# Optimization experiments

Measured on AMD Instinct MI355X. Metric: run time of the kernel, lower is better.

## Reference

```python
import jax, jax.numpy as jnp
import numpy as np

B, S, D, H = 1, 2048, 1024, 16
DH = D // H  # 64
ROPE_THETA = 10000.0


def _rope_tables(seq_len, half_dim, theta):
    inv = 1.0 / (theta ** (np.arange(0, half_dim, dtype=np.float32) / half_dim))
    ang = np.arange(seq_len, dtype=np.float32)[:, None] * inv[None, :]
    return jnp.asarray(np.cos(ang)), jnp.asarray(np.sin(ang))


def setup_inputs() -> dict:
    key = jax.random.key(0)
    ks = jax.random.split(key, 6)
    x = jax.random.normal(ks[0], (B, S, D), dtype=jnp.float32)
    # block-diagonal mask over ~4 packed images -> sorted segment ids
    seg_ids = jnp.sort(jax.random.randint(ks[1], (S,), 0, 4, dtype=jnp.int32))
    freqs_cos, freqs_sin = _rope_tables(S, DH // 2, ROPE_THETA)
    scale = 1.0 / np.sqrt(D)
    wq = jax.random.normal(ks[2], (D, D), dtype=jnp.float32) * scale
    wk = jax.random.normal(ks[3], (D, D), dtype=jnp.float32) * scale
    wv = jax.random.normal(ks[4], (D, D), dtype=jnp.float32) * scale
    wo = jax.random.normal(ks[5], (D, D), dtype=jnp.float32) * scale
    return {"x": x, "seg_ids": seg_ids, "freqs_cos": freqs_cos,
            "freqs_sin": freqs_sin, "wq": wq, "wk": wk, "wv": wv, "wo": wo}


def _apply_rope(t, cos, sin):
    # t: [B,S,H,DH]; interpret last dim as DH//2 complex pairs (real, imag)
    tr = t.reshape(B, S, H, DH // 2, 2)
    a, b = tr[..., 0], tr[..., 1]
    c = cos[None, :, None, :]  # [1,S,1,DH/2]
    s = sin[None, :, None, :]
    out = jnp.stack([a * c - b * s, a * s + b * c], axis=-1)
    return out.reshape(B, S, H, DH)


def reference(x, seg_ids, freqs_cos, freqs_sin, wq, wk, wv, wo):
    q = (x @ wq.T).reshape(B, S, H, DH)
    k = (x @ wk.T).reshape(B, S, H, DH)
    v = (x @ wv.T).reshape(B, S, H, DH)
    q = _apply_rope(q, freqs_cos, freqs_sin)
    k = _apply_rope(k, freqs_cos, freqs_sin)
    scores = jnp.einsum('bqhd,bkhd->bhqk', q, k) / np.float32(np.sqrt(DH))
    block_mask = (seg_ids[:, None] == seg_ids[None, :])  # [S,S] block-diagonal
    scores = jnp.where(block_mask[None, None], scores, jnp.float32(-1e9))
    attn = jax.nn.softmax(scores, axis=-1)
    out = jnp.einsum('bhqk,bkhd->bqhd', attn, v).reshape(B, S, D)
    return out @ wo.T
```

## Files before the change

kernel.cpp:

```cpp
#include <hip/hip_runtime.h>

typedef __bf16 bf16;
typedef __bf16 bf16x4 __attribute__((ext_vector_type(4)));
typedef __bf16 bf16x8 __attribute__((ext_vector_type(8)));
typedef float  f32x4  __attribute__((ext_vector_type(4)));

#define S_LEN 2048
#define D_DIM 1024
#define NHEAD 16
#define DHEAD 64

__device__ __forceinline__ void async_cp16(const bf16* g, bf16* l) {
  __builtin_amdgcn_global_load_lds(
      (__attribute__((address_space(1))) void*)(void*)g,
      (__attribute__((address_space(3))) void*)l,
      16, 0, 0);
}

__global__ __launch_bounds__(256) void cvt_k(
    const float* __restrict__ x,  const float* __restrict__ w0,
    const float* __restrict__ w1, const float* __restrict__ w2,
    const float* __restrict__ w3, bf16* __restrict__ dst,
    const int* __restrict__ seg, int* __restrict__ kbr)
{
  __shared__ int firstv[4];
  const int b = blockIdx.x;
  const int t = threadIdx.x;

  if (b < 3072) {
    int i = b * 256 + t;
    const float* src;
    int off;
    if (i < (1 << 18)) {
      src = x; off = i;
    } else {
      int j = i - (1 << 18);
      int s = j >> 17;
      off = j & ((1 << 17) - 1);
      src = (s == 0) ? w0 : (s == 1) ? w1 : (s == 2) ? w2 : w3;
    }
    f32x4 a = *(const f32x4*)(src + (size_t)off * 8);
    f32x4 bb = *(const f32x4*)(src + (size_t)off * 8 + 4);
    bf16x8 o;
    o[0] = (bf16)a[0];  o[1] = (bf16)a[1];  o[2] = (bf16)a[2];  o[3] = (bf16)a[3];
    o[4] = (bf16)bb[0]; o[5] = (bf16)bb[1]; o[6] = (bf16)bb[2]; o[7] = (bf16)bb[3];
    *((bf16x8*)dst + i) = o;
  } else {
    if (t < 4) firstv[t] = S_LEN;
    __syncthreads();
    for (int i = t; i < S_LEN; i += 256) {
      int s = seg[i];
      if (i == 0 || seg[i - 1] != s) atomicMin(&firstv[s], i);
    }
    __syncthreads();
    if (t < 32) {
      int smin = seg[t * 64], smax = seg[t * 64 + 63];
      int lb = S_LEN, ub = S_LEN;
      for (int vv = smin; vv < 4; ++vv) lb = min(lb, firstv[vv]);
      for (int vv = smax + 1; vv < 4; ++vv) ub = min(ub, firstv[vv]);
      kbr[t * 2] = lb >> 6;
      kbr[t * 2 + 1] = (ub - 1) >> 6;
    }
  }
}

__global__ __launch_bounds__(256) void gemm_qkv(
    const bf16* __restrict__ A,
    const bf16* __restrict__ B0, const bf16* __restrict__ B1,
    const bf16* __restrict__ B2,
    const float* __restrict__ cosT, const float* __restrict__ sinT,
    bf16* __restrict__ Cbase, bf16* __restrict__ Vt)
{
  constexpr int K = 1024, N = 1024;
  const int z = blockIdx.z;
  const bf16* W = (z == 0) ? B0 : (z == 1) ? B1 : B2;
  bf16* C = Cbase + (size_t)z * 2048 * 1024;

  __shared__ bf16 As[4][128 * 32] __attribute__((aligned(16)));
  __shared__ bf16 Bs[4][64 * 32] __attribute__((aligned(16)));

  const int t = threadIdx.x;
  const int lane = t & 63;
  const int w = t >> 6;
  const int lm = lane & 15, lq = lane >> 4;
  const int wr = w >> 1, wc = w & 1;
  const int bm = blockIdx.y, bn = blockIdx.x;

  const bf16* Abase = A + (size_t)bm * 128 * K;
  const bf16* Wbase = W + (size_t)bn * 64 * K;

  f32x4 acc[4][2] = {};

  for (int kk = 0; kk < K; kk += 128) {
#pragma unroll
    for (int kh = 0; kh < 2; ++kh)
#pragma unroll
      for (int g = 0; g < 2; ++g) {
        int c = (w * 2 + g) * 64 + lane;
        int row = c >> 2, k8 = c & 3;
        const bf16* ga = Abase + (size_t)row * K + kk + kh * 64 + k8 * 8;
        async_cp16(ga, &As[kh * 2][(w * 2 + g) * 512]);
        async_cp16(ga + 32, &As[kh * 2 + 1][(w * 2 + g) * 512]);
      }
#pragma unroll
    for (int kh = 0; kh < 2; ++kh) {
      int c = w * 64 + lane;
      int row = c >> 2, k8 = c & 3;
      const bf16* gb = Wbase + (size_t)row * K + kk + kh * 64 + k8 * 8;
      async_cp16(gb, &Bs[kh * 2][w * 512]);
      async_cp16(gb + 32, &Bs[kh * 2 + 1][w * 512]);
    }
    __syncthreads();

#pragma unroll
    for (int ks = 0; ks < 4; ++ks) {
      bf16x8 af[4], bfr[2];
#pragma unroll
      for (int mi = 0; mi < 4; ++mi)
        af[mi] = *(const bf16x8*)&As[ks][(wr * 64 + mi * 16 + lm) * 32 + lq * 8];
#pragma unroll
      for (int ni = 0; ni < 2; ++ni)
        bfr[ni] = *(const bf16x8*)&Bs[ks][(wc * 32 + ni * 16 + lm) * 32 + lq * 8];
#pragma unroll
      for (int mi = 0; mi < 4; ++mi)
#pragma unroll
        for (int ni = 0; ni < 2; ++ni)
          acc[mi][ni] = __builtin_amdgcn_mfma_f32_16x16x32_bf16(
              af[mi], bfr[ni], acc[mi][ni], 0, 0, 0);
    }
    __syncthreads();
  }

  if (z < 2) {
    const float scale = (z == 0) ? 0.125f : 1.0f;
#pragma unroll
    for (int mi = 0; mi < 4; ++mi)
#pragma unroll
      for (int ni = 0; ni < 2; ++ni) {
        int gcol = bn * 64 + wc * 32 + ni * 16 + lm;
        int p = (gcol & 63) >> 1;
        bool even = (gcol & 1) == 0;
#pragma unroll
        for (int r = 0; r < 4; ++r) {
          int row = bm * 128 + wr * 64 + mi * 16 + lq * 4 + r;
          float v = acc[mi][ni][r];
          float mate = __shfl_xor(v, 1);
          float cv = cosT[row * 32 + p];
          float sv = sinT[row * 32 + p];
          float res = even ? (v * cv - mate * sv) : (mate * sv + v * cv);
          C[(size_t)row * N + gcol] = (bf16)(res * scale);
        }
      }
  } else {
#pragma unroll
    for (int mi = 0; mi < 4; ++mi)
#pragma unroll
      for (int ni = 0; ni < 2; ++ni) {
        int gcol = bn * 64 + wc * 32 + ni * 16 + lm;
        int rowb = bm * 128 + wr * 64 + mi * 16 + lq * 4;
        bf16x4 pack;
#pragma unroll
        for (int r = 0; r < 4; ++r) pack[r] = (bf16)acc[mi][ni][r];
        *(bf16x4*)(Vt + (size_t)gcol * S_LEN + rowb) = pack;
      }
  }
}

__global__ __launch_bounds__(256) void gemm_wo(
    const bf16* __restrict__ A, const bf16* __restrict__ W,
    float* __restrict__ C)
{
  constexpr int K = 1024, N = 1024;

  __shared__ bf16 As[4][64 * 32] __attribute__((aligned(16)));
  __shared__ bf16 Bs[4][64 * 32] __attribute__((aligned(16)));

  const int t = threadIdx.x;
  const int lane = t & 63;
  const int w = t >> 6;
  const int lm = lane & 15, lq = lane >> 4;
  const int bn = blockIdx.x, bm = blockIdx.y;

  const bf16* Abase = A + (size_t)bm * 64 * K;
  const bf16* Wbase = W + (size_t)bn * 64 * K;

  f32x4 acc[4] = {};

  for (int kk = 0; kk < K; kk += 128) {
#pragma unroll
    for (int kh = 0; kh < 2; ++kh) {
      int c = w * 64 + lane;
      int row = c >> 2, k8 = c & 3;
      const bf16* ga = Abase + (size_t)row * K + kk + kh * 64 + k8 * 8;
      async_cp16(ga, &As[kh * 2][w * 512]);
      async_cp16(ga + 32, &As[kh * 2 + 1][w * 512]);
      const bf16* gb = Wbase + (size_t)row * K + kk + kh * 64 + k8 * 8;
      async_cp16(gb, &Bs[kh * 2][w * 512]);
      async_cp16(gb + 32, &Bs[kh * 2 + 1][w * 512]);
    }
    __syncthreads();

#pragma unroll
    for (int ks = 0; ks < 4; ++ks) {
      bf16x8 af = *(const bf16x8*)&As[ks][(w * 16 + lm) * 32 + lq * 8];
      bf16x8 bfr[4];
#pragma unroll
      for (int ni = 0; ni < 4; ++ni)
        bfr[ni] = *(const bf16x8*)&Bs[ks][(ni * 16 + lm) * 32 + lq * 8];
#pragma unroll
      for (int ni = 0; ni < 4; ++ni)
        acc[ni] = __builtin_amdgcn_mfma_f32_16x16x32_bf16(
            af, bfr[ni], acc[ni], 0, 0, 0);
    }
    __syncthreads();
  }

#pragma unroll
  for (int ni = 0; ni < 4; ++ni) {
    int col = bn * 64 + ni * 16 + lm;
#pragma unroll
    for (int r = 0; r < 4; ++r) {
      int row = bm * 64 + w * 16 + lq * 4 + r;
      C[(size_t)row * N + col] = acc[ni][r];
    }
  }
}

__global__ __launch_bounds__(512, 2) void attn_k(
    const bf16* __restrict__ Q, const bf16* __restrict__ Kmat,
    const bf16* __restrict__ Vt, const int* __restrict__ seg,
    const int* __restrict__ kbr,
    bf16* __restrict__ AO)
{
  __shared__ bf16 Ks[64 * 72] __attribute__((aligned(16)));
  __shared__ bf16 Vs[64 * 72] __attribute__((aligned(16)));
  __shared__ bf16 Ps[8][16 * 72] __attribute__((aligned(16)));
  __shared__ int segk[64];

  const int h = blockIdx.y;
  const int qt = blockIdx.x;
  const int q0 = qt * 128;
  const int t = threadIdx.x, lane = t & 63, w = t >> 6;
  const int lm = lane & 15, lq = lane >> 4;
  const int qrow = q0 + w * 16;

  const int kb0f = kbr[qt * 4], kb1f = kbr[qt * 4 + 3];

  bf16x8 qf[2];
#pragma unroll
  for (int ks = 0; ks < 2; ++ks)
    qf[ks] = *(const bf16x8*)(Q + (size_t)(qrow + lm) * D_DIM + h * DHEAD +
                              ks * 32 + lq * 8);

  int sq[4];
  float l_i[4];
#pragma unroll
  for (int r = 0; r < 4; ++r) {
    sq[r] = seg[qrow + lq * 4 + r];
    l_i[r] = 0.0f;
  }
  f32x4 o[4] = {};

  const int srow0 = t >> 3, sch = (t & 7) * 8;

  f32x4 pk0, pv0;
  int psg;
  {
    const int k0 = kb0f * 64;
    pk0 = *(const f32x4*)(Kmat + (size_t)(k0 + srow0) * D_DIM + h * DHEAD + sch);
    pv0 = *(const f32x4*)(Vt + (size_t)(h * DHEAD + srow0) * S_LEN + k0 + sch);
    if (t < 64) psg = seg[k0 + t];
  }

  for (int kb = kb0f; kb <= kb1f; ++kb) {
    __syncthreads();
    *(f32x4*)&Ks[srow0 * 72 + sch] = pk0;
    *(f32x4*)&Vs[srow0 * 72 + sch] = pv0;
    if (t < 64) segk[t] = psg;
    __syncthreads();

    if (kb + 1 <= kb1f) {
      const int k0 = (kb + 1) * 64;
      pk0 = *(const f32x4*)(Kmat + (size_t)(k0 + srow0) * D_DIM + h * DHEAD + sch);
      pv0 = *(const f32x4*)(Vt + (size_t)(h * DHEAD + srow0) * S_LEN + k0 + sch);
      if (t < 64) psg = seg[k0 + t];
    }

    f32x4 sa[4] = {};
    __builtin_amdgcn_s_setprio(1);
#pragma unroll
    for (int ks = 0; ks < 2; ++ks) {
      bf16x8 kf[4];
#pragma unroll
      for (int ni = 0; ni < 4; ++ni)
        kf[ni] = *(const bf16x8*)&Ks[(ni * 16 + lm) * 72 + ks * 32 + lq * 8];
#pragma unroll
      for (int ni = 0; ni < 4; ++ni)
        sa[ni] = __builtin_amdgcn_mfma_f32_16x16x32_bf16(qf[ks], kf[ni],
                                                         sa[ni], 0, 0, 0);
    }
    __builtin_amdgcn_s_setprio(0);

    int sk[4];
#pragma unroll
    for (int ni = 0; ni < 4; ++ni) sk[ni] = segk[ni * 16 + lm];

#pragma unroll
    for (int r = 0; r < 4; ++r)
#pragma unroll
      for (int ni = 0; ni < 4; ++ni) {
        float p = (sq[r] == sk[ni]) ? __expf(sa[ni][r]) : 0.0f;
        l_i[r] += p;
        Ps[w][(lq * 4 + r) * 72 + ni * 16 + lm] = (bf16)p;
      }

    __builtin_amdgcn_s_setprio(1);
#pragma unroll
    for (int ks = 0; ks < 2; ++ks) {
      bf16x8 pf = *(const bf16x8*)&Ps[w][lm * 72 + ks * 32 + lq * 8];
      bf16x8 vf[4];
#pragma unroll
      for (int ni = 0; ni < 4; ++ni)
        vf[ni] = *(const bf16x8*)&Vs[(ni * 16 + lm) * 72 + ks * 32 + lq * 8];
#pragma unroll
      for (int ni = 0; ni < 4; ++ni)
        o[ni] = __builtin_amdgcn_mfma_f32_16x16x32_bf16(pf, vf[ni], o[ni],
                                                        0, 0, 0);
    }
    __builtin_amdgcn_s_setprio(0);
  }

#pragma unroll
  for (int r = 0; r < 4; ++r) {
    float l = l_i[r];
    l += __shfl_xor(l, 1);
    l += __shfl_xor(l, 2);
    l += __shfl_xor(l, 4);
    l += __shfl_xor(l, 8);
    float inv = 1.0f / l;
    int row = qrow + lq * 4 + r;
#pragma unroll
    for (int ni = 0; ni < 4; ++ni)
      AO[(size_t)row * D_DIM + h * DHEAD + ni * 16 + lm] =
          (bf16)(o[ni][r] * inv);
  }
}

extern "C" void kernel_launch(void* const* d_in, const int* in_sizes, int n_in,
                              void* d_out, int out_size, void* d_ws,
                              size_t ws_size, hipStream_t stream)
{
  const float* x  = (const float*)d_in[0];
  const int*   sg = (const int*)d_in[1];
  const float* fc = (const float*)d_in[2];
  const float* fs = (const float*)d_in[3];
  const float* wq = (const float*)d_in[4];
  const float* wk = (const float*)d_in[5];
  const float* wv = (const float*)d_in[6];
  const float* wo = (const float*)d_in[7];
  float* out = (float*)d_out;

  const size_t MAT = (size_t)S_LEN * D_DIM;
  const size_t WSZ = (size_t)D_DIM * D_DIM;
  bf16* xb  = (bf16*)d_ws;
  bf16* wqb = xb + MAT;
  bf16* wkb = wqb + WSZ;
  bf16* wvb = wkb + WSZ;
  bf16* wob = wvb + WSZ;
  bf16* q0  = wob + WSZ;
  bf16* k0  = q0 + MAT;
  bf16* vt  = k0 + MAT;
  bf16* ao  = vt + MAT;
  int*  kbr = (int*)(ao + MAT);

  dim3 blk(256);
  cvt_k<<<dim3(3073), blk, 0, stream>>>(x, wq, wk, wv, wo, xb, sg, kbr);
  gemm_qkv<<<dim3(16, 16, 3), blk, 0, stream>>>(xb, wqb, wkb, wvb, fc, fs,
                                                q0, vt);
  attn_k<<<dim3(16, 16), dim3(512), 0, stream>>>(q0, k0, vt, sg, kbr, ao);
  gemm_wo<<<dim3(16, 32), blk, 0, stream>>>(ao, wob, out);
}
```

Measured before the change: 136.8 us.

## Give each attention wave two query sub-tiles and mask by key segment ranges

The attention kernel drops from 512 to 256 threads per block, and each wave now handles 32 query rows as two 16-row sub-tiles. Each K/V fragment read from LDS is reused across two sets of MFMAs. The score MFMA swaps its operand order so P comes out transposed, which allows packed bf16x4 stores into LDS. The per-key segment comparison is replaced by a key-index range test, using per-segment bounds computed in the convert kernel, so the segk shared array and its loads go away. The costs are higher register pressure, lower wave count per block, and an extra shuffle to redistribute the row normaliser.

```diff
diff --git a/kernel.cpp b/kernel.cpp
--- a/kernel.cpp
+++ b/kernel.cpp
@@ -61,6 +61,12 @@
       kbr[t * 2] = lb >> 6;
       kbr[t * 2 + 1] = (ub - 1) >> 6;
     }
+    if (t < 4) {
+      int ubv = S_LEN;
+      for (int u = t + 1; u < 4; ++u) ubv = min(ubv, firstv[u]);
+      kbr[64 + t * 2] = firstv[t];
+      kbr[64 + t * 2 + 1] = ubv;
+    }
   }
 }
 
@@ -226,7 +232,7 @@
   }
 }
 
-__global__ __launch_bounds__(512, 2) void attn_k(
+__global__ __launch_bounds__(256) void attn_k(
     const bf16* __restrict__ Q, const bf16* __restrict__ Kmat,
     const bf16* __restrict__ Vt, const int* __restrict__ seg,
     const int* __restrict__ kbr,
@@ -234,59 +240,63 @@
 {
   __shared__ bf16 Ks[64 * 72] __attribute__((aligned(16)));
   __shared__ bf16 Vs[64 * 72] __attribute__((aligned(16)));
-  __shared__ bf16 Ps[8][16 * 72] __attribute__((aligned(16)));
-  __shared__ int segk[64];
+  __shared__ bf16 Ps[4][2][16 * 72] __attribute__((aligned(16)));
 
   const int h = blockIdx.y;
   const int qt = blockIdx.x;
-  const int q0 = qt * 128;
   const int t = threadIdx.x, lane = t & 63, w = t >> 6;
   const int lm = lane & 15, lq = lane >> 4;
-  const int qrow = q0 + w * 16;
+  const int qbase = qt * 128 + w * 32;
 
   const int kb0f = kbr[qt * 4], kb1f = kbr[qt * 4 + 3];
 
-  bf16x8 qf[2];
-#pragma unroll
-  for (int ks = 0; ks < 2; ++ks)
-    qf[ks] = *(const bf16x8*)(Q + (size_t)(qrow + lm) * D_DIM + h * DHEAD +
-                              ks * 32 + lq * 8);
-
-  int sq[4];
-  float l_i[4];
-#pragma unroll
-  for (int r = 0; r < 4; ++r) {
-    sq[r] = seg[qrow + lq * 4 + r];
-    l_i[r] = 0.0f;
-  }
-  f32x4 o[4] = {};
-
-  const int srow0 = t >> 3, sch = (t & 7) * 8;
-
-  f32x4 pk0, pv0;
-  int psg;
+  bf16x8 qf[2][2];
+  int lb[2], ub[2];
+  float lacc[2] = {0.f, 0.f};
+  f32x4 o[2][4] = {};
+#pragma unroll
+  for (int s = 0; s < 2; ++s) {
+    int qrow = qbase + s * 16 + lm;
+#pragma unroll
+    for (int ks = 0; ks < 2; ++ks)
+      qf[s][ks] = *(const bf16x8*)(Q + (size_t)qrow * D_DIM + h * DHEAD +
+                                   ks * 32 + lq * 8);
+    int sv = seg[qrow];
+    lb[s] = kbr[64 + sv * 2];
+    ub[s] = kbr[64 + sv * 2 + 1];
+  }
+
+  const int srow0 = t >> 3, srow1 = srow0 + 32;
+  const int sch = (t & 7) * 8;
+
+  f32x4 pk0, pk1, pv0, pv1;
   {
     const int k0 = kb0f * 64;
     pk0 = *(const f32x4*)(Kmat + (size_t)(k0 + srow0) * D_DIM + h * DHEAD + sch);
+    pk1 = *(const f32x4*)(Kmat + (size_t)(k0 + srow1) * D_DIM + h * DHEAD + sch);
     pv0 = *(const f32x4*)(Vt + (size_t)(h * DHEAD + srow0) * S_LEN + k0 + sch);
-    if (t < 64) psg = seg[k0 + t];
+    pv1 = *(const f32x4*)(Vt + (size_t)(h * DHEAD + srow1) * S_LEN + k0 + sch);
   }
 
   for (int kb = kb0f; kb <= kb1f; ++kb) {
     __syncthreads();
     *(f32x4*)&Ks[srow0 * 72 + sch] = pk0;
+    *(f32x4*)&Ks[srow1 * 72 + sch] = pk1;
     *(f32x4*)&Vs[srow0 * 72 + sch] = pv0;
-    if (t < 64) segk[t] = psg;
-    __syncthreads();
-
-    if (kb + 1 <= kb1f) {
+    *(f32x4*)&Vs[srow1 * 72 + sch] = pv1;
+    __syncthreads();
+
+    if (kb < kb1f) {
       const int k0 = (kb + 1) * 64;
       pk0 = *(const f32x4*)(Kmat + (size_t)(k0 + srow0) * D_DIM + h * DHEAD + sch);
+      pk1 = *(const f32x4*)(Kmat + (size_t)(k0 + srow1) * D_DIM + h * DHEAD + sch);
       pv0 = *(const f32x4*)(Vt + (size_t)(h * DHEAD + srow0) * S_LEN + k0 + sch);
-      if (t < 64) psg = seg[k0 + t];
-    }
-
-    f32x4 sa[4] = {};
+      pv1 = *(const f32x4*)(Vt + (size_t)(h * DHEAD + srow1) * S_LEN + k0 + sch);
+    }
+
+    const int k0 = kb * 64;
+
+    f32x4 sa[2][4] = {};
     __builtin_amdgcn_s_setprio(1);
 #pragma unroll
     for (int ks = 0; ks < 2; ++ks) {
@@ -295,54 +305,63 @@
       for (int ni = 0; ni < 4; ++ni)
         kf[ni] = *(const bf16x8*)&Ks[(ni * 16 + lm) * 72 + ks * 32 + lq * 8];
 #pragma unroll
-      for (int ni = 0; ni < 4; ++ni)
-        sa[ni] = __builtin_amdgcn_mfma_f32_16x16x32_bf16(qf[ks], kf[ni],
-                                                         sa[ni], 0, 0, 0);
+      for (int s = 0; s < 2; ++s)
+#pragma unroll
+        for (int ni = 0; ni < 4; ++ni)
+          sa[s][ni] = __builtin_amdgcn_mfma_f32_16x16x32_bf16(
+              kf[ni], qf[s][ks], sa[s][ni], 0, 0, 0);
     }
     __builtin_amdgcn_s_setprio(0);
 
-    int sk[4];
-#pragma unroll
-    for (int ni = 0; ni < 4; ++ni) sk[ni] = segk[ni * 16 + lm];
-
-#pragma unroll
-    for (int r = 0; r < 4; ++r)
+#pragma unroll
+    for (int s = 0; s < 2; ++s)
 #pragma unroll
       for (int ni = 0; ni < 4; ++ni) {
-        float p = (sq[r] == sk[ni]) ? __expf(sa[ni][r]) : 0.0f;
-        l_i[r] += p;
-        Ps[w][(lq * 4 + r) * 72 + ni * 16 + lm] = (bf16)p;
+        bf16x4 pk;
+#pragma unroll
+        for (int r = 0; r < 4; ++r) {
+          int key = k0 + ni * 16 + lq * 4 + r;
+          float p = (key >= lb[s] && key < ub[s]) ? __expf(sa[s][ni][r]) : 0.0f;
+          lacc[s] += p;
+          pk[r] = (bf16)p;
+        }
+        *(bf16x4*)&Ps[w][s][lm * 72 + ni * 16 + lq * 4] = pk;
       }
 
     __builtin_amdgcn_s_setprio(1);
 #pragma unroll
     for (int ks = 0; ks < 2; ++ks) {
-      bf16x8 pf = *(const bf16x8*)&Ps[w][lm * 72 + ks * 32 + lq * 8];
       bf16x8 vf[4];
 #pragma unroll
       for (int ni = 0; ni < 4; ++ni)
         vf[ni] = *(const bf16x8*)&Vs[(ni * 16 + lm) * 72 + ks * 32 + lq * 8];
 #pragma unroll
+      for (int s = 0; s < 2; ++s) {
+        bf16x8 pf = *(const bf16x8*)&Ps[w][s][lm * 72 + ks * 32 + lq * 8];
+#pragma unroll
+        for (int ni = 0; ni < 4; ++ni)
+          o[s][ni] = __builtin_amdgcn_mfma_f32_16x16x32_bf16(
+              pf, vf[ni], o[s][ni], 0, 0, 0);
+      }
+    }
+    __builtin_amdgcn_s_setprio(0);
+  }
+
+#pragma unroll
+  for (int s = 0; s < 2; ++s) {
+    float l = lacc[s];
+    l += __shfl_xor(l, 16);
+    l += __shfl_xor(l, 32);
+    float inv = 1.0f / l;
+#pragma unroll
+    for (int r = 0; r < 4; ++r) {
+      float invr = __shfl(inv, lq * 4 + r);
+      int row = qbase + s * 16 + lq * 4 + r;
+#pragma unroll
       for (int ni = 0; ni < 4; ++ni)
-        o[ni] = __builtin_amdgcn_mfma_f32_16x16x32_bf16(pf, vf[ni], o[ni],
-                                                        0, 0, 0);
-    }
-    __builtin_amdgcn_s_setprio(0);
-  }
-
-#pragma unroll
-  for (int r = 0; r < 4; ++r) {
-    float l = l_i[r];
-    l += __shfl_xor(l, 1);
-    l += __shfl_xor(l, 2);
-    l += __shfl_xor(l, 4);
-    l += __shfl_xor(l, 8);
-    float inv = 1.0f / l;
-    int row = qrow + lq * 4 + r;
-#pragma unroll
-    for (int ni = 0; ni < 4; ++ni)
-      AO[(size_t)row * D_DIM + h * DHEAD + ni * 16 + lm] =
-          (bf16)(o[ni][r] * inv);
+        AO[(size_t)row * D_DIM + h * DHEAD + ni * 16 + lm] =
+            (bf16)(o[s][ni][r] * invr);
+    }
   }
 }
 
@@ -377,6 +396,6 @@
   cvt_k<<<dim3(3073), blk, 0, stream>>>(x, wq, wk, wv, wo, xb, sg, kbr);
   gemm_qkv<<<dim3(16, 16, 3), blk, 0, stream>>>(xb, wqb, wkb, wvb, fc, fs,
                                                 q0, vt);
-  attn_k<<<dim3(16, 16), dim3(512), 0, stream>>>(q0, k0, vt, sg, kbr, ao);
+  attn_k<<<dim3(16, 16), blk, 0, stream>>>(q0, k0, vt, sg, kbr, ao);
   gemm_wo<<<dim3(16, 32), blk, 0, stream>>>(ao, wob, out);
 }
```

Result: slower. 143.6 us (+5.0%).

## Load K/V fragments directly from global and mask by segment range bounds

Applied to the files above, without the earlier changes.

Removes the shared-memory staging of K and V tiles and the two block barriers per key block; each wave now loads its MFMA operand fragments straight from global memory. The segment-equality mask is replaced by a per-query-row key range [lb, ub) precomputed in the conversion kernel, which removes the segk LDS array. This trades barrier and LDS traffic for redundant global/L2 loads across the 8 waves and loses the register prefetch of the next tile.

```diff
diff --git a/kernel.cpp b/kernel.cpp
--- a/kernel.cpp
+++ b/kernel.cpp
@@ -61,6 +61,12 @@
       kbr[t * 2] = lb >> 6;
       kbr[t * 2 + 1] = (ub - 1) >> 6;
     }
+    if (t < 4) {
+      int ubv = S_LEN;
+      for (int u = t + 1; u < 4; ++u) ubv = min(ubv, firstv[u]);
+      kbr[64 + t * 2] = firstv[t];
+      kbr[64 + t * 2 + 1] = ubv;
+    }
   }
 }
 
@@ -232,10 +238,7 @@
     const int* __restrict__ kbr,
     bf16* __restrict__ AO)
 {
-  __shared__ bf16 Ks[64 * 72] __attribute__((aligned(16)));
-  __shared__ bf16 Vs[64 * 72] __attribute__((aligned(16)));
   __shared__ bf16 Ps[8][16 * 72] __attribute__((aligned(16)));
-  __shared__ int segk[64];
 
   const int h = blockIdx.y;
   const int qt = blockIdx.x;
@@ -252,39 +255,22 @@
     qf[ks] = *(const bf16x8*)(Q + (size_t)(qrow + lm) * D_DIM + h * DHEAD +
                               ks * 32 + lq * 8);
 
-  int sq[4];
+  int lbq[4], ubq[4];
   float l_i[4];
 #pragma unroll
   for (int r = 0; r < 4; ++r) {
-    sq[r] = seg[qrow + lq * 4 + r];
+    int sv = seg[qrow + lq * 4 + r];
+    lbq[r] = kbr[64 + sv * 2];
+    ubq[r] = kbr[64 + sv * 2 + 1];
     l_i[r] = 0.0f;
   }
   f32x4 o[4] = {};
 
-  const int srow0 = t >> 3, sch = (t & 7) * 8;
-
-  f32x4 pk0, pv0;
-  int psg;
-  {
-    const int k0 = kb0f * 64;
-    pk0 = *(const f32x4*)(Kmat + (size_t)(k0 + srow0) * D_DIM + h * DHEAD + sch);
-    pv0 = *(const f32x4*)(Vt + (size_t)(h * DHEAD + srow0) * S_LEN + k0 + sch);
-    if (t < 64) psg = seg[k0 + t];
-  }
+  const bf16* Kb = Kmat + h * DHEAD;
+  const bf16* Vb = Vt + (size_t)h * DHEAD * S_LEN;
 
   for (int kb = kb0f; kb <= kb1f; ++kb) {
-    __syncthreads();
-    *(f32x4*)&Ks[srow0 * 72 + sch] = pk0;
-    *(f32x4*)&Vs[srow0 * 72 + sch] = pv0;
-    if (t < 64) segk[t] = psg;
-    __syncthreads();
-
-    if (kb + 1 <= kb1f) {
-      const int k0 = (kb + 1) * 64;
-      pk0 = *(const f32x4*)(Kmat + (size_t)(k0 + srow0) * D_DIM + h * DHEAD + sch);
-      pv0 = *(const f32x4*)(Vt + (size_t)(h * DHEAD + srow0) * S_LEN + k0 + sch);
-      if (t < 64) psg = seg[k0 + t];
-    }
+    const int k0 = kb * 64;
 
     f32x4 sa[4] = {};
     __builtin_amdgcn_s_setprio(1);
@@ -293,7 +279,8 @@
       bf16x8 kf[4];
 #pragma unroll
       for (int ni = 0; ni < 4; ++ni)
-        kf[ni] = *(const bf16x8*)&Ks[(ni * 16 + lm) * 72 + ks * 32 + lq * 8];
+        kf[ni] = *(const bf16x8*)(Kb + (size_t)(k0 + ni * 16 + lm) * D_DIM +
+                                  ks * 32 + lq * 8);
 #pragma unroll
       for (int ni = 0; ni < 4; ++ni)
         sa[ni] = __builtin_amdgcn_mfma_f32_16x16x32_bf16(qf[ks], kf[ni],
@@ -301,15 +288,12 @@
     }
     __builtin_amdgcn_s_setprio(0);
 
-    int sk[4];
-#pragma unroll
-    for (int ni = 0; ni < 4; ++ni) sk[ni] = segk[ni * 16 + lm];
-
 #pragma unroll
     for (int r = 0; r < 4; ++r)
 #pragma unroll
       for (int ni = 0; ni < 4; ++ni) {
-        float p = (sq[r] == sk[ni]) ? __expf(sa[ni][r]) : 0.0f;
+        int key = k0 + ni * 16 + lm;
+        float p = (key >= lbq[r] && key < ubq[r]) ? __expf(sa[ni][r]) : 0.0f;
         l_i[r] += p;
         Ps[w][(lq * 4 + r) * 72 + ni * 16 + lm] = (bf16)p;
       }
@@ -321,7 +305,8 @@
       bf16x8 vf[4];
 #pragma unroll
       for (int ni = 0; ni < 4; ++ni)
-        vf[ni] = *(const bf16x8*)&Vs[(ni * 16 + lm) * 72 + ks * 32 + lq * 8];
+        vf[ni] = *(const bf16x8*)(Vb + (size_t)(ni * 16 + lm) * S_LEN +
+                                  k0 + ks * 32 + lq * 8);
 #pragma unroll
       for (int ni = 0; ni < 4; ++ni)
         o[ni] = __builtin_amdgcn_mfma_f32_16x16x32_bf16(pf, vf[ni], o[ni],
```

After: 180.2 us. 31.7% more time.

## Transpose QK^T MFMA output and replace segment-id lookup with key range bounds

Applied to the files above, without the earlier changes.

Swaps the MFMA operands so each lane holds scores for one query row across four consecutive keys. Per-key segment-id loads into shared memory become a comparison against precomputed per-segment [start,end) bounds, which rely on segment ids being sorted. P is written to shared memory as packed 4-wide bf16 stores instead of scalar stores, and the row-sum reduction needs fewer shuffles. The cost is an extra shuffle per row to redistribute the inverse normaliser at the end.

```diff
diff --git a/kernel.cpp b/kernel.cpp
--- a/kernel.cpp
+++ b/kernel.cpp
@@ -61,6 +61,12 @@
       kbr[t * 2] = lb >> 6;
       kbr[t * 2 + 1] = (ub - 1) >> 6;
     }
+    if (t < 4) {
+      int ubv = S_LEN;
+      for (int u = t + 1; u < 4; ++u) ubv = min(ubv, firstv[u]);
+      kbr[64 + t * 2] = firstv[t];
+      kbr[64 + t * 2 + 1] = ubv;
+    }
   }
 }
 
@@ -235,7 +241,6 @@
   __shared__ bf16 Ks[64 * 72] __attribute__((aligned(16)));
   __shared__ bf16 Vs[64 * 72] __attribute__((aligned(16)));
   __shared__ bf16 Ps[8][16 * 72] __attribute__((aligned(16)));
-  __shared__ int segk[64];
 
   const int h = blockIdx.y;
   const int qt = blockIdx.x;
@@ -252,39 +257,37 @@
     qf[ks] = *(const bf16x8*)(Q + (size_t)(qrow + lm) * D_DIM + h * DHEAD +
                               ks * 32 + lq * 8);
 
-  int sq[4];
-  float l_i[4];
-#pragma unroll
-  for (int r = 0; r < 4; ++r) {
-    sq[r] = seg[qrow + lq * 4 + r];
-    l_i[r] = 0.0f;
-  }
+  int lb, ub;
+  {
+    int sv = seg[qrow + lm];
+    lb = kbr[64 + sv * 2];
+    ub = kbr[64 + sv * 2 + 1];
+  }
+  float lacc = 0.0f;
   f32x4 o[4] = {};
 
   const int srow0 = t >> 3, sch = (t & 7) * 8;
 
   f32x4 pk0, pv0;
-  int psg;
   {
     const int k0 = kb0f * 64;
     pk0 = *(const f32x4*)(Kmat + (size_t)(k0 + srow0) * D_DIM + h * DHEAD + sch);
     pv0 = *(const f32x4*)(Vt + (size_t)(h * DHEAD + srow0) * S_LEN + k0 + sch);
-    if (t < 64) psg = seg[k0 + t];
   }
 
   for (int kb = kb0f; kb <= kb1f; ++kb) {
     __syncthreads();
     *(f32x4*)&Ks[srow0 * 72 + sch] = pk0;
     *(f32x4*)&Vs[srow0 * 72 + sch] = pv0;
-    if (t < 64) segk[t] = psg;
     __syncthreads();
 
     if (kb + 1 <= kb1f) {
       const int k0 = (kb + 1) * 64;
       pk0 = *(const f32x4*)(Kmat + (size_t)(k0 + srow0) * D_DIM + h * DHEAD + sch);
       pv0 = *(const f32x4*)(Vt + (size_t)(h * DHEAD + srow0) * S_LEN + k0 + sch);
-      if (t < 64) psg = seg[k0 + t];
-    }
+    }
+
+    const int k0 = kb * 64;
 
     f32x4 sa[4] = {};
     __builtin_amdgcn_s_setprio(1);
@@ -296,23 +299,23 @@
         kf[ni] = *(const bf16x8*)&Ks[(ni * 16 + lm) * 72 + ks * 32 + lq * 8];
 #pragma unroll
       for (int ni = 0; ni < 4; ++ni)
-        sa[ni] = __builtin_amdgcn_mfma_f32_16x16x32_bf16(qf[ks], kf[ni],
+        sa[ni] = __builtin_amdgcn_mfma_f32_16x16x32_bf16(kf[ni], qf[ks],
                                                          sa[ni], 0, 0, 0);
     }
     __builtin_amdgcn_s_setprio(0);
 
-    int sk[4];
-#pragma unroll
-    for (int ni = 0; ni < 4; ++ni) sk[ni] = segk[ni * 16 + lm];
-
-#pragma unroll
-    for (int r = 0; r < 4; ++r)
-#pragma unroll
-      for (int ni = 0; ni < 4; ++ni) {
-        float p = (sq[r] == sk[ni]) ? __expf(sa[ni][r]) : 0.0f;
-        l_i[r] += p;
-        Ps[w][(lq * 4 + r) * 72 + ni * 16 + lm] = (bf16)p;
+#pragma unroll
+    for (int ni = 0; ni < 4; ++ni) {
+      bf16x4 pk;
+#pragma unroll
+      for (int r = 0; r < 4; ++r) {
+        int key = k0 + ni * 16 + lq * 4 + r;
+        float p = (key >= lb && key < ub) ? __expf(sa[ni][r]) : 0.0f;
+        lacc += p;
+        pk[r] = (bf16)p;
       }
+      *(bf16x4*)&Ps[w][lm * 72 + ni * 16 + lq * 4] = pk;
+    }
 
     __builtin_amdgcn_s_setprio(1);
 #pragma unroll
@@ -330,19 +333,20 @@
     __builtin_amdgcn_s_setprio(0);
   }
 
-#pragma unroll
-  for (int r = 0; r < 4; ++r) {
-    float l = l_i[r];
-    l += __shfl_xor(l, 1);
-    l += __shfl_xor(l, 2);
-    l += __shfl_xor(l, 4);
-    l += __shfl_xor(l, 8);
+  {
+    float l = lacc;
+    l += __shfl_xor(l, 16);
+    l += __shfl_xor(l, 32);
     float inv = 1.0f / l;
-    int row = qrow + lq * 4 + r;
-#pragma unroll
-    for (int ni = 0; ni < 4; ++ni)
-      AO[(size_t)row * D_DIM + h * DHEAD + ni * 16 + lm] =
-          (bf16)(o[ni][r] * inv);
+#pragma unroll
+    for (int r = 0; r < 4; ++r) {
+      float invr = __shfl(inv, lq * 4 + r);
+      int row = qrow + lq * 4 + r;
+#pragma unroll
+      for (int ni = 0; ni < 4; ++ni)
+        AO[(size_t)row * D_DIM + h * DHEAD + ni * 16 + lm] =
+            (bf16)(o[ni][r] * invr);
+    }
   }
 }
 
```

Measured after the change: 137.7 us. Within noise of the previous version (+0.7%).
